# Kernel optimization log

Hardware: AMD Instinct MI355X
Metric: run time of the kernel (lower is better)

## Reference

```python
import jax, jax.numpy as jnp
import numpy as np

N_NODES = 100000
H_FEATS = 256
N_EDGES = 300000
NUM_CLASSES = 1


def setup_inputs() -> dict:
    key = jax.random.key(0)
    k1, k2, k3, k4, k5 = jax.random.split(key, 5)
    x = jax.random.normal(k1, (N_NODES, H_FEATS), dtype=jnp.float32)
    edge_index = jax.random.randint(k2, (2, N_EDGES), 0, N_NODES, dtype=jnp.int64)
    # MLP params (stored as [in, out] for x @ W + b)
    in1 = 2 * H_FEATS
    W1 = jax.random.normal(k3, (in1, H_FEATS), dtype=jnp.float32) / np.sqrt(in1)
    b1 = jnp.zeros((H_FEATS,), dtype=jnp.float32)
    W2 = jax.random.normal(k4, (H_FEATS, NUM_CLASSES), dtype=jnp.float32) / np.sqrt(H_FEATS)
    b2 = jnp.zeros((NUM_CLASSES,), dtype=jnp.float32)
    return {"x": x, "edge_index": edge_index, "W1": W1, "b1": b1, "W2": W2, "b2": b2}


def reference(x, edge_index, W1, b1, W2, b2):
    # Gather source/dest node embeddings and concat -> [E, 2*h_feats]
    h = jnp.concatenate([x[edge_index[0]], x[edge_index[1]]], axis=-1)
    h = jax.nn.relu(h @ W1 + b1)          # [E, h_feats]
    h = h @ W2 + b2                        # [E, num_classes]
    return jnp.squeeze(h, axis=1)          # [E]
```

## Files before the change

### kernel.cpp

```cpp
#include <hip/hip_runtime.h>
#include <hip/hip_bf16.h>

#define NN 100000
#define H  256
#define NE 300000
#define KOUT 512
#define MT  782

typedef __attribute__((ext_vector_type(8))) short short8;
typedef __attribute__((ext_vector_type(8))) unsigned short ushort8v;
typedef __attribute__((ext_vector_type(4))) float f32x4;

__device__ __forceinline__ unsigned short f2bf(float f) {
    unsigned int u = __float_as_uint(f);
    u += 0x7FFFu + ((u >> 16) & 1u);
    return (unsigned short)(u >> 16);
}
__device__ __forceinline__ float bf2f(unsigned short h) {
    return __uint_as_float(((unsigned int)h) << 16);
}
__device__ __forceinline__ int swz(int row, int coloff) {
    return row * 128 + (coloff ^ ((row & 7) << 4));
}
__device__ __forceinline__ void gload16(const void* g, void* l) {
    __builtin_amdgcn_global_load_lds((const __attribute__((address_space(1))) void*)g,
                                     (__attribute__((address_space(3))) void*)l,
                                     16, 0, 0);
}

__global__ __launch_bounds__(256) void wprep(const float* __restrict__ W1,
                                             unsigned short* __restrict__ wsB) {
    int gtid = blockIdx.x * 256 + threadIdx.x;
    int t  = gtid >> 10;
    int kg = (gtid >> 7) & 7;
    int n  = gtid & 127;
    int ks = t >> 2, nt = t & 3;
    int krow0 = ks * 64 + kg * 8 + ((nt >= 2) ? 256 : 0);
    int col = (nt & 1) * 128 + n;
    const float* src = W1 + (size_t)krow0 * 256 + col;
    ushort8v p;
    #pragma unroll
    for (int i = 0; i < 8; ++i) p[i] = f2bf(src[(size_t)i * 256]);
    *(ushort8v*)((char*)(wsB + t * 8192) + swz(n, kg * 16)) = p;
}

__global__ __launch_bounds__(1024, 4) void gemm_f(const float* __restrict__ x,
                                                  const unsigned short* __restrict__ wsB,
                                                  unsigned short* __restrict__ y) {
    __shared__ unsigned short Al[8192];
    __shared__ unsigned short Bl[32768];
    const int tid = threadIdx.x;
    const int m0 = (int)blockIdx.x * 128;
    const int lane = tid & 63, wid = tid >> 6;
    const int wm = (wid >> 3) * 64;
    const int wn = (wid & 7) * 64;
    const int lr = lane & 15, lk = lane >> 4;

    const int ar = tid >> 3, acg = tid & 7;
    int node_s = m0 + ar; if (node_s > NN - 1) node_s = NN - 1;
    const float* xs = x + (size_t)node_s * H + acg * 8;

    const char* bs = (const char*)wsB + wid * 4096 + lane * 16;
    char* bd = (char*)Bl + wid * 4096;

    float4 p0, p1;
    f32x4 acc[4][4] = {};

    p0 = *(const float4*)(xs);
    p1 = *(const float4*)(xs + 4);

    #pragma unroll
    for (int ks = 0; ks < 4; ++ks) {
        if (ks) __syncthreads();
        #pragma unroll
        for (int i = 0; i < 4; ++i)
            gload16(bs + ks * 65536 + i * 1024, bd + i * 1024);
        {
            ushort8v q;
            q[0] = f2bf(p0.x); q[1] = f2bf(p0.y); q[2] = f2bf(p0.z); q[3] = f2bf(p0.w);
            q[4] = f2bf(p1.x); q[5] = f2bf(p1.y); q[6] = f2bf(p1.z); q[7] = f2bf(p1.w);
            *(ushort8v*)((char*)Al + swz(ar, acg * 16)) = q;
        }
        __syncthreads();
        if (ks < 3) {
            p0 = *(const float4*)(xs + (ks + 1) * 64);
            p1 = *(const float4*)(xs + (ks + 1) * 64 + 4);
        }
        #pragma unroll
        for (int kk = 0; kk < 64; kk += 32) {
            const int coloff = kk * 2 + lk * 16;
            short8 a[4], b[4];
            #pragma unroll
            for (int mi = 0; mi < 4; ++mi)
                a[mi] = *(const short8*)((const char*)Al + swz(wm + mi * 16 + lr, coloff));
            #pragma unroll
            for (int ni = 0; ni < 4; ++ni) {
                const int f = wn + ni * 16 + lr;
                b[ni] = *(const short8*)((const char*)Bl + (f >> 7) * 16384 + swz(f & 127, coloff));
            }
            #pragma unroll
            for (int ni = 0; ni < 4; ++ni)
                #pragma unroll
                for (int mi = 0; mi < 4; ++mi)
                    acc[ni][mi] = __builtin_amdgcn_mfma_f32_16x16x32_bf16(b[ni], a[mi], acc[ni][mi], 0, 0, 0);
        }
    }
    #pragma unroll
    for (int mi = 0; mi < 4; ++mi) {
        const int node = m0 + wm + mi * 16 + lr;
        if (node < NN) {
            #pragma unroll
            for (int ni = 0; ni < 4; ++ni) {
                const int feat = wn + ni * 16 + lk * 4;
                ushort4 u;
                u.x = f2bf(acc[ni][mi][0]);
                u.y = f2bf(acc[ni][mi][1]);
                u.z = f2bf(acc[ni][mi][2]);
                u.w = f2bf(acc[ni][mi][3]);
                *(ushort4*)(y + (size_t)node * KOUT + feat) = u;
            }
        }
    }
}

__global__ __launch_bounds__(256) void edge_v2(const unsigned short* __restrict__ y,
                                               const int* __restrict__ ei,
                                               const float* __restrict__ b1,
                                               const float* __restrict__ W2,
                                               const float* __restrict__ b2,
                                               float* __restrict__ out) {
    const int tid = threadIdx.x;
    const int l32 = tid & 31;
    const int ghw = ((int)(blockIdx.x * blockDim.x) + tid) >> 5;
    const int nhw = ((int)(gridDim.x * blockDim.x)) >> 5;
    const int j = l32 * 8;
    const float4 b01 = *(const float4*)(b1 + j);
    const float4 b23 = *(const float4*)(b1 + j + 4);
    const float4 w01 = *(const float4*)(W2 + j);
    const float4 w23 = *(const float4*)(W2 + j + 4);
    const float bb = b2[0];
    #pragma unroll 2
    for (int e = ghw; e < NE; e += nhw) {
        int s = ei[e], d = ei[NE + e];
        s = s < 0 ? 0 : (s > NN - 1 ? NN - 1 : s);
        d = d < 0 ? 0 : (d > NN - 1 ? NN - 1 : d);
        ushort8v us = *(const ushort8v*)(y + (size_t)s * KOUT + j);
        ushort8v ud = *(const ushort8v*)(y + (size_t)d * KOUT + 256 + j);
        float acc;
        acc  = fmaxf(bf2f(us[0]) + bf2f(ud[0]) + b01.x, 0.f) * w01.x;
        acc += fmaxf(bf2f(us[1]) + bf2f(ud[1]) + b01.y, 0.f) * w01.y;
        acc += fmaxf(bf2f(us[2]) + bf2f(ud[2]) + b01.z, 0.f) * w01.z;
        acc += fmaxf(bf2f(us[3]) + bf2f(ud[3]) + b01.w, 0.f) * w01.w;
        acc += fmaxf(bf2f(us[4]) + bf2f(ud[4]) + b23.x, 0.f) * w23.x;
        acc += fmaxf(bf2f(us[5]) + bf2f(ud[5]) + b23.y, 0.f) * w23.y;
        acc += fmaxf(bf2f(us[6]) + bf2f(ud[6]) + b23.z, 0.f) * w23.z;
        acc += fmaxf(bf2f(us[7]) + bf2f(ud[7]) + b23.w, 0.f) * w23.w;
        #pragma unroll
        for (int off = 16; off > 0; off >>= 1) acc += __shfl_xor(acc, off, 64);
        if (l32 == 0) out[e] = acc + bb;
    }
}

__global__ __launch_bounds__(256) void fused_fallback(const float* __restrict__ x,
                                                      const int* __restrict__ ei,
                                                      const float* __restrict__ W1,
                                                      const float* __restrict__ b1,
                                                      const float* __restrict__ W2,
                                                      const float* __restrict__ b2,
                                                      float* __restrict__ out) {
    __shared__ float xsh[4][512];
    const int lane = threadIdx.x & 63;
    const int wl = threadIdx.x >> 6;
    const int gw = (blockIdx.x * blockDim.x + threadIdx.x) >> 6;
    const int nw = (gridDim.x * blockDim.x) >> 6;
    const int j = lane * 4;
    const float4 bv = *(const float4*)(b1 + j);
    const float4 wv = *(const float4*)(W2 + j);
    const float bb = b2[0];
    for (int e = gw; e < NE; e += nw) {
        int s = ei[e], d = ei[NE + e];
        s = min(max(s, 0), NN - 1);
        d = min(max(d, 0), NN - 1);
        __threadfence_block();
        #pragma unroll
        for (int i = 0; i < 4; ++i) {
            xsh[wl][i * 64 + lane]       = x[(size_t)s * H + i * 64 + lane];
            xsh[wl][256 + i * 64 + lane] = x[(size_t)d * H + i * 64 + lane];
        }
        __threadfence_block();
        float h0 = bv.x, h1 = bv.y, h2 = bv.z, h3 = bv.w;
        for (int k = 0; k < 256; ++k) {
            float xa = xsh[wl][k], xb2 = xsh[wl][256 + k];
            float4 wa = *(const float4*)(W1 + (size_t)k * 256 + j);
            float4 wb = *(const float4*)(W1 + (size_t)(k + 256) * 256 + j);
            h0 += xa * wa.x + xb2 * wb.x;
            h1 += xa * wa.y + xb2 * wb.y;
            h2 += xa * wa.z + xb2 * wb.z;
            h3 += xa * wa.w + xb2 * wb.w;
        }
        float acc = fmaxf(h0, 0.f) * wv.x + fmaxf(h1, 0.f) * wv.y +
                    fmaxf(h2, 0.f) * wv.z + fmaxf(h3, 0.f) * wv.w;
        #pragma unroll
        for (int off = 32; off > 0; off >>= 1) acc += __shfl_xor(acc, off, 64);
        if (lane == 0) out[e] = acc + bb;
    }
}

extern "C" void kernel_launch(void* const* d_in, const int* in_sizes, int n_in,
                              void* d_out, int out_size, void* d_ws, size_t ws_size,
                              hipStream_t stream) {
    const float* x  = (const float*)d_in[0];
    const int*   ei = (const int*)d_in[1];
    const float* W1 = (const float*)d_in[2];
    const float* b1 = (const float*)d_in[3];
    const float* W2 = (const float*)d_in[4];
    const float* b2 = (const float*)d_in[5];
    float* out = (float*)d_out;

    const size_t ybytes = (size_t)NN * KOUT * sizeof(unsigned short);
    const size_t wbytes = 16 * 8192 * sizeof(unsigned short);

    if (ws_size >= ybytes + wbytes) {
        unsigned short* yb = (unsigned short*)d_ws;
        unsigned short* wb = (unsigned short*)((char*)d_ws + ybytes);
        wprep<<<dim3(64), dim3(256), 0, stream>>>(W1, wb);
        gemm_f<<<dim3(MT), dim3(1024), 0, stream>>>(x, wb, yb);
        edge_v2<<<dim3(2048), dim3(256), 0, stream>>>(yb, ei, b1, W2, b2, out);
    } else {
        fused_fallback<<<dim3(2048), dim3(256), 0, stream>>>(x, ei, W1, b1, W2, b2, out);
    }
}
```

Before: 122.9 us.

## Make node-feature GEMM persistent with weight N-tile resident in LDS

The per-node GEMM becomes a persistent kernel of 256 blocks. Each block loads one 128-column slice of the bf16 weights into LDS once, then loops over 64-row node chunks. Node rows are converted to bf16 into a double-buffered LDS A tile, and the next chunk is prefetched into registers while MFMAs run. The aim is to stop each block from reloading the full weight matrix and to overlap x loads with compute. In exchange, every x row is now read by four blocks (one per column slice), and the large LDS footprint with 256-thread blocks lowers occupancy.

```diff
diff --git a/kernel.cpp b/kernel.cpp
--- a/kernel.cpp
+++ b/kernel.cpp
@@ -5,7 +5,7 @@
 #define H  256
 #define NE 300000
 #define KOUT 512
-#define MT  782
+#define MT64 1563
 
 typedef __attribute__((ext_vector_type(8))) short short8;
 typedef __attribute__((ext_vector_type(8))) unsigned short ushort8v;
@@ -34,7 +34,7 @@
     int t  = gtid >> 10;
     int kg = (gtid >> 7) & 7;
     int n  = gtid & 127;
-    int ks = t >> 2, nt = t & 3;
+    int nt = t >> 2, ks = t & 3;
     int krow0 = ks * 64 + kg * 8 + ((nt >= 2) ? 256 : 0);
     int col = (nt & 1) * 128 + n;
     const float* src = W1 + (size_t)krow0 * 256 + col;
@@ -44,80 +44,100 @@
     *(ushort8v*)((char*)(wsB + t * 8192) + swz(n, kg * 16)) = p;
 }
 
-__global__ __launch_bounds__(1024, 4) void gemm_f(const float* __restrict__ x,
-                                                  const unsigned short* __restrict__ wsB,
-                                                  unsigned short* __restrict__ y) {
-    __shared__ unsigned short Al[8192];
+__global__ __launch_bounds__(256) void gemm_v5(const float* __restrict__ x,
+                                               const unsigned short* __restrict__ wsB,
+                                               unsigned short* __restrict__ y) {
     __shared__ unsigned short Bl[32768];
+    __shared__ unsigned short Al[32768];
     const int tid = threadIdx.x;
-    const int m0 = (int)blockIdx.x * 128;
+    const int nt = (int)blockIdx.x & 3;
+    const int chunk = (int)blockIdx.x >> 2;
     const int lane = tid & 63, wid = tid >> 6;
-    const int wm = (wid >> 3) * 64;
-    const int wn = (wid & 7) * 64;
+    const int wm = (wid & 1) * 32;
+    const int wn = (wid >> 1) * 64;
     const int lr = lane & 15, lk = lane >> 4;
 
-    const int ar = tid >> 3, acg = tid & 7;
-    int node_s = m0 + ar; if (node_s > NN - 1) node_s = NN - 1;
-    const float* xs = x + (size_t)node_s * H + acg * 8;
-
-    const char* bs = (const char*)wsB + wid * 4096 + lane * 16;
-    char* bd = (char*)Bl + wid * 4096;
-
-    float4 p0, p1;
-    f32x4 acc[4][4] = {};
-
-    p0 = *(const float4*)(xs);
-    p1 = *(const float4*)(xs + 4);
-
-    #pragma unroll
-    for (int ks = 0; ks < 4; ++ks) {
-        if (ks) __syncthreads();
-        #pragma unroll
-        for (int i = 0; i < 4; ++i)
-            gload16(bs + ks * 65536 + i * 1024, bd + i * 1024);
+    {
+        const char* bs = (const char*)wsB + nt * 65536 + wid * 1024 + lane * 16;
+        char* bd = (char*)Bl + wid * 1024;
+        #pragma unroll
+        for (int r = 0; r < 16; ++r)
+            gload16(bs + r * 4096, bd + r * 4096);
+    }
+
+    const int arow = tid >> 2;
+    const int kseg = tid & 3;
+    const int niters = (MT64 + 63 - chunk) >> 6;
+
+    float4 pA[16];
+    {
+        int node = chunk * 64 + arow; if (node > NN - 1) node = NN - 1;
+        const float* xp = x + (size_t)node * H + kseg * 64;
+        #pragma unroll
+        for (int q = 0; q < 16; ++q) pA[q] = *(const float4*)(xp + q * 4);
+    }
+
+    for (int i = 0; i < niters; ++i) {
+        const int abase = (i & 1) * 32768;
         {
-            ushort8v q;
-            q[0] = f2bf(p0.x); q[1] = f2bf(p0.y); q[2] = f2bf(p0.z); q[3] = f2bf(p0.w);
-            q[4] = f2bf(p1.x); q[5] = f2bf(p1.y); q[6] = f2bf(p1.z); q[7] = f2bf(p1.w);
-            *(ushort8v*)((char*)Al + swz(ar, acg * 16)) = q;
+            char* ab = (char*)Al + abase + kseg * 8192;
+            #pragma unroll
+            for (int g = 0; g < 8; ++g) {
+                ushort8v q;
+                q[0] = f2bf(pA[2*g].x);   q[1] = f2bf(pA[2*g].y);
+                q[2] = f2bf(pA[2*g].z);   q[3] = f2bf(pA[2*g].w);
+                q[4] = f2bf(pA[2*g+1].x); q[5] = f2bf(pA[2*g+1].y);
+                q[6] = f2bf(pA[2*g+1].z); q[7] = f2bf(pA[2*g+1].w);
+                *(ushort8v*)(ab + swz(arow, g * 16)) = q;
+            }
         }
         __syncthreads();
-        if (ks < 3) {
-            p0 = *(const float4*)(xs + (ks + 1) * 64);
-            p1 = *(const float4*)(xs + (ks + 1) * 64 + 4);
-        }
-        #pragma unroll
-        for (int kk = 0; kk < 64; kk += 32) {
-            const int coloff = kk * 2 + lk * 16;
-            short8 a[4], b[4];
-            #pragma unroll
-            for (int mi = 0; mi < 4; ++mi)
-                a[mi] = *(const short8*)((const char*)Al + swz(wm + mi * 16 + lr, coloff));
-            #pragma unroll
-            for (int ni = 0; ni < 4; ++ni) {
-                const int f = wn + ni * 16 + lr;
-                b[ni] = *(const short8*)((const char*)Bl + (f >> 7) * 16384 + swz(f & 127, coloff));
-            }
+        if (i + 1 < niters) {
+            int node = (chunk + (i + 1) * 64) * 64 + arow;
+            if (node > NN - 1) node = NN - 1;
+            const float* xp = x + (size_t)node * H + kseg * 64;
+            #pragma unroll
+            for (int q = 0; q < 16; ++q) pA[q] = *(const float4*)(xp + q * 4);
+        }
+        f32x4 acc[4][2];
+        #pragma unroll
+        for (int ni = 0; ni < 4; ++ni)
+            #pragma unroll
+            for (int mi = 0; mi < 2; ++mi) acc[ni][mi] = (f32x4){0.f, 0.f, 0.f, 0.f};
+        #pragma unroll
+        for (int st = 0; st < 8; ++st) {
+            const int ksub = st >> 1;
+            const int coloff = (st & 1) * 64 + lk * 16;
+            short8 a[2], b[4];
+            #pragma unroll
+            for (int mi = 0; mi < 2; ++mi)
+                a[mi] = *(const short8*)((const char*)Al + abase + ksub * 8192 +
+                                         swz(wm + mi * 16 + lr, coloff));
+            #pragma unroll
+            for (int ni = 0; ni < 4; ++ni)
+                b[ni] = *(const short8*)((const char*)Bl + ksub * 16384 +
+                                         swz(wn + ni * 16 + lr, coloff));
             #pragma unroll
             for (int ni = 0; ni < 4; ++ni)
                 #pragma unroll
-                for (int mi = 0; mi < 4; ++mi)
+                for (int mi = 0; mi < 2; ++mi)
                     acc[ni][mi] = __builtin_amdgcn_mfma_f32_16x16x32_bf16(b[ni], a[mi], acc[ni][mi], 0, 0, 0);
         }
-    }
-    #pragma unroll
-    for (int mi = 0; mi < 4; ++mi) {
-        const int node = m0 + wm + mi * 16 + lr;
-        if (node < NN) {
-            #pragma unroll
-            for (int ni = 0; ni < 4; ++ni) {
-                const int feat = wn + ni * 16 + lk * 4;
-                ushort4 u;
-                u.x = f2bf(acc[ni][mi][0]);
-                u.y = f2bf(acc[ni][mi][1]);
-                u.z = f2bf(acc[ni][mi][2]);
-                u.w = f2bf(acc[ni][mi][3]);
-                *(ushort4*)(y + (size_t)node * KOUT + feat) = u;
+        const int m0 = (chunk + i * 64) * 64;
+        #pragma unroll
+        for (int mi = 0; mi < 2; ++mi) {
+            const int node = m0 + wm + mi * 16 + lr;
+            if (node < NN) {
+                #pragma unroll
+                for (int ni = 0; ni < 4; ++ni) {
+                    const int feat = nt * 128 + wn + ni * 16 + lk * 4;
+                    ushort4 u;
+                    u.x = f2bf(acc[ni][mi][0]);
+                    u.y = f2bf(acc[ni][mi][1]);
+                    u.z = f2bf(acc[ni][mi][2]);
+                    u.w = f2bf(acc[ni][mi][3]);
+                    *(ushort4*)(y + (size_t)node * KOUT + feat) = u;
+                }
             }
         }
     }
@@ -224,7 +244,7 @@
         unsigned short* yb = (unsigned short*)d_ws;
         unsigned short* wb = (unsigned short*)((char*)d_ws + ybytes);
         wprep<<<dim3(64), dim3(256), 0, stream>>>(W1, wb);
-        gemm_f<<<dim3(MT), dim3(1024), 0, stream>>>(x, wb, yb);
+        gemm_v5<<<dim3(256), dim3(256), 0, stream>>>(x, wb, yb);
         edge_v2<<<dim3(2048), dim3(256), 0, stream>>>(yb, ei, b1, W2, b2, out);
     } else {
         fused_fallback<<<dim3(2048), dim3(256), 0, stream>>>(x, ei, W1, b1, W2, b2, out);
```

Measured after the change: 148.6 us. +20.9%, slower.

## Keep half of W1 resident in LDS and stream node strips per wave

Applied to the files above, without the earlier changes.

Replaces the 128-row tiled node GEMM with a persistent-style kernel. Each 512-thread block loads one 256-column half of the bf16 W1 (128 KB) into LDS once, then each wave processes 32-node strips, reading x straight from global into registers as the MFMA A operand with no LDS staging and no per-k-step barriers. Blocks are mapped so each XCD handles a contiguous range of node chunks, and the W1 prep layout is reordered to match. The cost is a large LDS footprint (one block per CU), 128 accumulator registers per lane, and each x row being read twice, once for each column half.

```diff
diff --git a/kernel.cpp b/kernel.cpp
--- a/kernel.cpp
+++ b/kernel.cpp
@@ -5,7 +5,6 @@
 #define H  256
 #define NE 300000
 #define KOUT 512
-#define MT  782
 
 typedef __attribute__((ext_vector_type(8))) short short8;
 typedef __attribute__((ext_vector_type(8))) unsigned short ushort8v;
@@ -26,6 +25,14 @@
     __builtin_amdgcn_global_load_lds((const __attribute__((address_space(1))) void*)g,
                                      (__attribute__((address_space(3))) void*)l,
                                      16, 0, 0);
+}
+__device__ __forceinline__ short8 pack8(float4 a, float4 b) {
+    short8 r;
+    r[0] = (short)f2bf(a.x); r[1] = (short)f2bf(a.y);
+    r[2] = (short)f2bf(a.z); r[3] = (short)f2bf(a.w);
+    r[4] = (short)f2bf(b.x); r[5] = (short)f2bf(b.y);
+    r[6] = (short)f2bf(b.z); r[7] = (short)f2bf(b.w);
+    return r;
 }
 
 __global__ __launch_bounds__(256) void wprep(const float* __restrict__ W1,
@@ -34,7 +41,7 @@
     int t  = gtid >> 10;
     int kg = (gtid >> 7) & 7;
     int n  = gtid & 127;
-    int ks = t >> 2, nt = t & 3;
+    int nt = t >> 2, ks = t & 3;
     int krow0 = ks * 64 + kg * 8 + ((nt >= 2) ? 256 : 0);
     int col = (nt & 1) * 128 + n;
     const float* src = W1 + (size_t)krow0 * 256 + col;
@@ -44,80 +51,92 @@
     *(ushort8v*)((char*)(wsB + t * 8192) + swz(n, kg * 16)) = p;
 }
 
-__global__ __launch_bounds__(1024, 4) void gemm_f(const float* __restrict__ x,
-                                                  const unsigned short* __restrict__ wsB,
-                                                  unsigned short* __restrict__ y) {
-    __shared__ unsigned short Al[8192];
-    __shared__ unsigned short Bl[32768];
+__global__ __launch_bounds__(512) void gemm_v7(const float* __restrict__ x,
+                                               const unsigned short* __restrict__ wsB,
+                                               unsigned short* __restrict__ y) {
+    __shared__ unsigned short Bl[65536];
     const int tid = threadIdx.x;
-    const int m0 = (int)blockIdx.x * 128;
     const int lane = tid & 63, wid = tid >> 6;
-    const int wm = (wid >> 3) * 64;
-    const int wn = (wid & 7) * 64;
-    const int lr = lane & 15, lk = lane >> 4;
-
-    const int ar = tid >> 3, acg = tid & 7;
-    int node_s = m0 + ar; if (node_s > NN - 1) node_s = NN - 1;
-    const float* xs = x + (size_t)node_s * H + acg * 8;
-
-    const char* bs = (const char*)wsB + wid * 4096 + lane * 16;
-    char* bd = (char*)Bl + wid * 4096;
-
-    float4 p0, p1;
-    f32x4 acc[4][4] = {};
-
-    p0 = *(const float4*)(xs);
-    p1 = *(const float4*)(xs + 4);
-
-    #pragma unroll
-    for (int ks = 0; ks < 4; ++ks) {
-        if (ks) __syncthreads();
-        #pragma unroll
-        for (int i = 0; i < 4; ++i)
-            gload16(bs + ks * 65536 + i * 1024, bd + i * 1024);
-        {
-            ushort8v q;
-            q[0] = f2bf(p0.x); q[1] = f2bf(p0.y); q[2] = f2bf(p0.z); q[3] = f2bf(p0.w);
-            q[4] = f2bf(p1.x); q[5] = f2bf(p1.y); q[6] = f2bf(p1.z); q[7] = f2bf(p1.w);
-            *(ushort8v*)((char*)Al + swz(ar, acg * 16)) = q;
-        }
-        __syncthreads();
-        if (ks < 3) {
-            p0 = *(const float4*)(xs + (ks + 1) * 64);
-            p1 = *(const float4*)(xs + (ks + 1) * 64 + 4);
-        }
-        #pragma unroll
-        for (int kk = 0; kk < 64; kk += 32) {
-            const int coloff = kk * 2 + lk * 16;
-            short8 a[4], b[4];
+    const int xcd = (int)blockIdx.x & 7;
+    const int jj  = (int)blockIdx.x >> 3;
+    const int nt2 = jj & 1;
+    const int chunk = xcd * 16 + (jj >> 1);
+
+    {
+        const char* bs = (const char*)wsB + nt2 * 131072 + wid * 16384 + lane * 16;
+        char* bd = (char*)Bl + wid * 16384;
+        #pragma unroll
+        for (int r = 0; r < 16; ++r)
+            gload16(bs + r * 1024, bd + r * 1024);
+    }
+    __syncthreads();
+
+    const int s0 = chunk * 782;
+    const int nstrips = min(25, (NN - s0 + 31) >> 5);
+    const int nlo = lane & 15, ksl = lane >> 4;
+    const int fbase = nt2 * 256 + ksl * 4;
+
+    for (int s = wid; s < nstrips; s += 8) {
+        const int nb = s0 + s * 32;
+        int n0 = nb + nlo;      if (n0 > NN - 1) n0 = NN - 1;
+        int n1 = nb + 16 + nlo; if (n1 > NN - 1) n1 = NN - 1;
+        const float* xp0 = x + (size_t)n0 * H + ksl * 8;
+        const float* xp1 = x + (size_t)n1 * H + ksl * 8;
+
+        f32x4 acc[16][2];
+        #pragma unroll
+        for (int ni = 0; ni < 16; ++ni)
             #pragma unroll
-            for (int mi = 0; mi < 4; ++mi)
-                a[mi] = *(const short8*)((const char*)Al + swz(wm + mi * 16 + lr, coloff));
+            for (int mi = 0; mi < 2; ++mi) acc[ni][mi] = (f32x4){0.f, 0.f, 0.f, 0.f};
+
+        float4 u0 = *(const float4*)(xp0);
+        float4 u1 = *(const float4*)(xp0 + 4);
+        float4 v0 = *(const float4*)(xp1);
+        float4 v1 = *(const float4*)(xp1 + 4);
+
+        #pragma unroll
+        for (int ks = 0; ks < 8; ++ks) {
+            short8 a0 = pack8(u0, u1);
+            short8 a1 = pack8(v0, v1);
+            if (ks < 7) {
+                u0 = *(const float4*)(xp0 + (ks + 1) * 32);
+                u1 = *(const float4*)(xp0 + (ks + 1) * 32 + 4);
+                v0 = *(const float4*)(xp1 + (ks + 1) * 32);
+                v1 = *(const float4*)(xp1 + (ks + 1) * 32 + 4);
+            }
+            const int boff = (ks >> 1) * 16384 + ((ks & 1) * 64 + ksl * 16 ^ 0);
             #pragma unroll
-            for (int ni = 0; ni < 4; ++ni) {
-                const int f = wn + ni * 16 + lr;
-                b[ni] = *(const short8*)((const char*)Bl + (f >> 7) * 16384 + swz(f & 127, coloff));
+            for (int nig = 0; nig < 4; ++nig) {
+                short8 b[4];
+                #pragma unroll
+                for (int t4 = 0; t4 < 4; ++t4) {
+                    const int ni = nig * 4 + t4;
+                    const int q = ni >> 3, fn = (ni & 7) * 16 + nlo;
+                    b[t4] = *(const short8*)((const char*)Bl + q * 65536 + (ks >> 1) * 16384 +
+                                             swz(fn, (ks & 1) * 64 + ksl * 16));
+                }
+                #pragma unroll
+                for (int t4 = 0; t4 < 4; ++t4) {
+                    const int ni = nig * 4 + t4;
+                    acc[ni][0] = __builtin_amdgcn_mfma_f32_16x16x32_bf16(b[t4], a0, acc[ni][0], 0, 0, 0);
+                    acc[ni][1] = __builtin_amdgcn_mfma_f32_16x16x32_bf16(b[t4], a1, acc[ni][1], 0, 0, 0);
+                }
             }
+            (void)boff;
+        }
+        #pragma unroll
+        for (int mi = 0; mi < 2; ++mi) {
+            int node = nb + mi * 16 + nlo;
+            if (node > NN - 1) node = NN - 1;
+            unsigned short* yp = y + (size_t)node * KOUT + fbase;
             #pragma unroll
-            for (int ni = 0; ni < 4; ++ni)
-                #pragma unroll
-                for (int mi = 0; mi < 4; ++mi)
-                    acc[ni][mi] = __builtin_amdgcn_mfma_f32_16x16x32_bf16(b[ni], a[mi], acc[ni][mi], 0, 0, 0);
-        }
-    }
-    #pragma unroll
-    for (int mi = 0; mi < 4; ++mi) {
-        const int node = m0 + wm + mi * 16 + lr;
-        if (node < NN) {
-            #pragma unroll
-            for (int ni = 0; ni < 4; ++ni) {
-                const int feat = wn + ni * 16 + lk * 4;
+            for (int ni = 0; ni < 16; ++ni) {
                 ushort4 u;
                 u.x = f2bf(acc[ni][mi][0]);
                 u.y = f2bf(acc[ni][mi][1]);
                 u.z = f2bf(acc[ni][mi][2]);
                 u.w = f2bf(acc[ni][mi][3]);
-                *(ushort4*)(y + (size_t)node * KOUT + feat) = u;
+                *(ushort4*)(yp + ni * 16) = u;
             }
         }
     }
@@ -224,7 +243,7 @@
         unsigned short* yb = (unsigned short*)d_ws;
         unsigned short* wb = (unsigned short*)((char*)d_ws + ybytes);
         wprep<<<dim3(64), dim3(256), 0, stream>>>(W1, wb);
-        gemm_f<<<dim3(MT), dim3(1024), 0, stream>>>(x, wb, yb);
+        gemm_v7<<<dim3(256), dim3(512), 0, stream>>>(x, wb, yb);
         edge_v2<<<dim3(2048), dim3(256), 0, stream>>>(yb, ei, b1, W2, b2, out);
     } else {
         fused_fallback<<<dim3(2048), dim3(256), 0, stream>>>(x, ei, W1, b1, W2, b2, out);
```

Measured after the change: 320.0 us. 160% more time.

## Pre-convert x to swizzled bf16 tiles and double-buffer a 128x128 GEMM

Applied to the files above, without the earlier changes.

Adds an xprep2 kernel that converts x to bf16 in the pre-swizzled tile layout, so the GEMM can load both A and B straight into LDS with global_load_lds. The GEMM moves from 1024-thread blocks that each compute 128x512 to 256-thread blocks that each compute 128x128. These blocks double-buffer LDS across the K steps and use a remapped block index for locality. The aim is to overlap loads with MFMA work and raise occupancy, at the cost of an extra kernel launch and an extra round trip of x through memory.

```diff
diff --git a/kernel.cpp b/kernel.cpp
--- a/kernel.cpp
+++ b/kernel.cpp
@@ -34,7 +34,7 @@
     int t  = gtid >> 10;
     int kg = (gtid >> 7) & 7;
     int n  = gtid & 127;
-    int ks = t >> 2, nt = t & 3;
+    int nt = t >> 2, ks = t & 3;
     int krow0 = ks * 64 + kg * 8 + ((nt >= 2) ? 256 : 0);
     int col = (nt & 1) * 128 + n;
     const float* src = W1 + (size_t)krow0 * 256 + col;
@@ -44,66 +44,84 @@
     *(ushort8v*)((char*)(wsB + t * 8192) + swz(n, kg * 16)) = p;
 }
 
-__global__ __launch_bounds__(1024, 4) void gemm_f(const float* __restrict__ x,
-                                                  const unsigned short* __restrict__ wsB,
-                                                  unsigned short* __restrict__ y) {
-    __shared__ unsigned short Al[8192];
-    __shared__ unsigned short Bl[32768];
+__global__ __launch_bounds__(512) void xprep2(const float* __restrict__ x,
+                                              unsigned short* __restrict__ xb) {
+    int gid = blockIdx.x * 512 + threadIdx.x;
+    int t   = gid >> 9;
+    int rem = gid & 511;
+    int r   = rem >> 2;
+    int gp  = (rem & 3) * 2;
+    int mt = t >> 2, ks = t & 3;
+    int node = mt * 128 + r; if (node > NN - 1) node = NN - 1;
+    const float* src = x + (size_t)node * H + ks * 64 + gp * 8;
+    float4 v0 = *(const float4*)(src);
+    float4 v1 = *(const float4*)(src + 4);
+    float4 v2 = *(const float4*)(src + 8);
+    float4 v3 = *(const float4*)(src + 12);
+    ushort8v p0, p1;
+    p0[0]=f2bf(v0.x); p0[1]=f2bf(v0.y); p0[2]=f2bf(v0.z); p0[3]=f2bf(v0.w);
+    p0[4]=f2bf(v1.x); p0[5]=f2bf(v1.y); p0[6]=f2bf(v1.z); p0[7]=f2bf(v1.w);
+    p1[0]=f2bf(v2.x); p1[1]=f2bf(v2.y); p1[2]=f2bf(v2.z); p1[3]=f2bf(v2.w);
+    p1[4]=f2bf(v3.x); p1[5]=f2bf(v3.y); p1[6]=f2bf(v3.z); p1[7]=f2bf(v3.w);
+    char* dst = (char*)(xb + (size_t)t * 8192);
+    *(ushort8v*)(dst + swz(r, gp * 16))      = p0;
+    *(ushort8v*)(dst + swz(r, gp * 16 + 16)) = p1;
+}
+
+__global__ __launch_bounds__(256) void gemm_v8(const unsigned short* __restrict__ xb,
+                                               const unsigned short* __restrict__ wsB,
+                                               unsigned short* __restrict__ y) {
+    __shared__ unsigned short Al[2][8192];
+    __shared__ unsigned short Bl[2][8192];
     const int tid = threadIdx.x;
-    const int m0 = (int)blockIdx.x * 128;
+    const int logical = ((int)blockIdx.x & 7) * ((int)gridDim.x >> 3) + ((int)blockIdx.x >> 3);
+    const int mt = logical >> 2, nt = logical & 3;
+    const int m0 = mt * 128, n0 = nt * 128;
     const int lane = tid & 63, wid = tid >> 6;
-    const int wm = (wid >> 3) * 64;
-    const int wn = (wid & 7) * 64;
+    const int wm = (wid >> 1) * 64, wn = (wid & 1) * 64;
     const int lr = lane & 15, lk = lane >> 4;
 
-    const int ar = tid >> 3, acg = tid & 7;
-    int node_s = m0 + ar; if (node_s > NN - 1) node_s = NN - 1;
-    const float* xs = x + (size_t)node_s * H + acg * 8;
-
-    const char* bs = (const char*)wsB + wid * 4096 + lane * 16;
-    char* bd = (char*)Bl + wid * 4096;
-
-    float4 p0, p1;
+    const char* asrc = (const char*)(xb + (size_t)mt * 4 * 8192) + wid * 4096 + lane * 16;
+    const char* bsrc = (const char*)(wsB + nt * 4 * 8192) + wid * 4096 + lane * 16;
+
     f32x4 acc[4][4] = {};
 
-    p0 = *(const float4*)(xs);
-    p1 = *(const float4*)(xs + 4);
+    #pragma unroll
+    for (int i = 0; i < 4; ++i) {
+        gload16(asrc + i * 1024, (char*)Al[0] + wid * 4096 + i * 1024);
+        gload16(bsrc + i * 1024, (char*)Bl[0] + wid * 4096 + i * 1024);
+    }
+    __syncthreads();
 
     #pragma unroll
     for (int ks = 0; ks < 4; ++ks) {
-        if (ks) __syncthreads();
-        #pragma unroll
-        for (int i = 0; i < 4; ++i)
-            gload16(bs + ks * 65536 + i * 1024, bd + i * 1024);
-        {
-            ushort8v q;
-            q[0] = f2bf(p0.x); q[1] = f2bf(p0.y); q[2] = f2bf(p0.z); q[3] = f2bf(p0.w);
-            q[4] = f2bf(p1.x); q[5] = f2bf(p1.y); q[6] = f2bf(p1.z); q[7] = f2bf(p1.w);
-            *(ushort8v*)((char*)Al + swz(ar, acg * 16)) = q;
-        }
-        __syncthreads();
         if (ks < 3) {
-            p0 = *(const float4*)(xs + (ks + 1) * 64);
-            p1 = *(const float4*)(xs + (ks + 1) * 64 + 4);
-        }
+            const int nb = (ks + 1) & 1;
+            #pragma unroll
+            for (int i = 0; i < 4; ++i) {
+                gload16(asrc + (ks + 1) * 16384 + i * 1024, (char*)Al[nb] + wid * 4096 + i * 1024);
+                gload16(bsrc + (ks + 1) * 16384 + i * 1024, (char*)Bl[nb] + wid * 4096 + i * 1024);
+            }
+        }
+        const char* Ab = (const char*)Al[ks & 1];
+        const char* Bb = (const char*)Bl[ks & 1];
         #pragma unroll
         for (int kk = 0; kk < 64; kk += 32) {
             const int coloff = kk * 2 + lk * 16;
             short8 a[4], b[4];
             #pragma unroll
             for (int mi = 0; mi < 4; ++mi)
-                a[mi] = *(const short8*)((const char*)Al + swz(wm + mi * 16 + lr, coloff));
-            #pragma unroll
-            for (int ni = 0; ni < 4; ++ni) {
-                const int f = wn + ni * 16 + lr;
-                b[ni] = *(const short8*)((const char*)Bl + (f >> 7) * 16384 + swz(f & 127, coloff));
-            }
+                a[mi] = *(const short8*)(Ab + swz(wm + mi * 16 + lr, coloff));
+            #pragma unroll
+            for (int ni = 0; ni < 4; ++ni)
+                b[ni] = *(const short8*)(Bb + swz(wn + ni * 16 + lr, coloff));
             #pragma unroll
             for (int ni = 0; ni < 4; ++ni)
                 #pragma unroll
                 for (int mi = 0; mi < 4; ++mi)
                     acc[ni][mi] = __builtin_amdgcn_mfma_f32_16x16x32_bf16(b[ni], a[mi], acc[ni][mi], 0, 0, 0);
         }
+        __syncthreads();
     }
     #pragma unroll
     for (int mi = 0; mi < 4; ++mi) {
@@ -111,7 +129,7 @@
         if (node < NN) {
             #pragma unroll
             for (int ni = 0; ni < 4; ++ni) {
-                const int feat = wn + ni * 16 + lk * 4;
+                const int feat = n0 + wn + ni * 16 + lk * 4;
                 ushort4 u;
                 u.x = f2bf(acc[ni][mi][0]);
                 u.y = f2bf(acc[ni][mi][1]);
@@ -217,14 +235,17 @@
     const float* b2 = (const float*)d_in[5];
     float* out = (float*)d_out;
 
-    const size_t ybytes = (size_t)NN * KOUT * sizeof(unsigned short);
-    const size_t wbytes = 16 * 8192 * sizeof(unsigned short);
-
-    if (ws_size >= ybytes + wbytes) {
-        unsigned short* yb = (unsigned short*)d_ws;
-        unsigned short* wb = (unsigned short*)((char*)d_ws + ybytes);
+    const size_t ybytes  = (size_t)NN * KOUT * sizeof(unsigned short);
+    const size_t xbbytes = (size_t)MT * 4 * 16384;
+    const size_t wbytes  = 16 * 8192 * sizeof(unsigned short);
+
+    if (ws_size >= ybytes + xbbytes + wbytes) {
+        unsigned short* yb  = (unsigned short*)d_ws;
+        unsigned short* xbb = (unsigned short*)((char*)d_ws + ybytes);
+        unsigned short* wb  = (unsigned short*)((char*)d_ws + ybytes + xbbytes);
         wprep<<<dim3(64), dim3(256), 0, stream>>>(W1, wb);
-        gemm_f<<<dim3(MT), dim3(1024), 0, stream>>>(x, wb, yb);
+        xprep2<<<dim3(MT * 4), dim3(512), 0, stream>>>(x, xbb);
+        gemm_v8<<<dim3(MT * 4), dim3(256), 0, stream>>>(xbb, wb, yb);
         edge_v2<<<dim3(2048), dim3(256), 0, stream>>>(yb, ei, b1, W2, b2, out);
     } else {
         fused_fallback<<<dim3(2048), dim3(256), 0, stream>>>(x, ei, W1, b1, W2, b2, out);
```

Result: slower. 135.4 us (+10.1%).
